# Kernel tuning notes

Hardware: AMD Instinct MI355X
Metric: run time of the kernel (lower is better)

## Reference

```python
import jax, jax.numpy as jnp
import numpy as np

SIGNAL = (32, 32)
KERNEL = (8, 8)
N_FEATURES = [64, 128, 128]
BATCH = 64
ALPHA = 0.5          # source references an undefined global `alpha`; fixed here
LEAKY_SLOPE = 0.01   # torch F.leaky_relu default


def _join_tensor(S, K, loc):
    i = np.arange(S)[:, None, None]
    j = np.arange(S)[None, :, None]
    k = np.arange(K)[None, None, :]
    M = (j >= i) & (i == np.maximum(j, k + loc))
    return jnp.asarray(M.astype(np.float32))


def _meet_tensor(S, K, loc):
    i = np.arange(S)[:, None, None]
    j = np.arange(S)[None, :, None]
    k = np.arange(K)[None, None, :]
    M = (j >= i) & (i == np.minimum(j, k + loc))
    return jnp.asarray(M.astype(np.float32))


def setup_inputs() -> dict:
    key = jax.random.key(0)
    sx, sy = SIGNAL
    kx, ky = KERNEL
    # meet layers use kernel_loc = signal - kernel; join layers use (0, 0)
    cmx = _meet_tensor(sx, kx, sx - kx)
    cmy = _meet_tensor(sy, ky, sy - ky)
    cjx = _join_tensor(sx, kx, 0)
    cjy = _join_tensor(sy, ky, 0)

    keys = jax.random.split(key, 16)
    x = jax.random.normal(keys[0], (BATCH, N_FEATURES[0], sx, sy), dtype=jnp.float32)

    def kaiming(k, shape):
        fan_in = shape[0] * shape[1] * shape[2]  # kx*ky*in_features
        return jax.random.normal(k, shape, dtype=jnp.float32) * np.float32(np.sqrt(2.0 / fan_in))

    inp = {"x": x, "cmx": cmx, "cmy": cmy, "cjx": cjx, "cjy": cjy}
    for li in range(len(N_FEATURES) - 1):
        fi, fo = N_FEATURES[li], N_FEATURES[li + 1]
        inp[f"mw{li}"] = kaiming(keys[1 + 2 * li], (kx, ky, fi, fo))
        inp[f"mb{li}"] = jnp.zeros((fo, 1, 1), dtype=jnp.float32)
        inp[f"jw{li}"] = kaiming(keys[2 + 2 * li], (kx, ky, fi, fo))
        inp[f"jb{li}"] = jnp.zeros((fo, 1, 1), dtype=jnp.float32)
    return inp


def _lattice_conv(cx, cy, X, W, b):
    # Y[m,g,x,y] = sum_{i,j,a,b} cx[i,x,a] cy[j,y,b] X[m,f,i,j] W[a,b,f,g] + bias
    return jnp.einsum('ixa,jyb,mfij,abfg->mgxy', cx, cy, X, W, optimize='optimal') + b


def reference(x, cmx, cmy, cjx, cjy, mw0, mb0, jw0, jb0, mw1, mb1, jw1, jb1):
    params = [(mw0, mb0, jw0, jb0), (mw1, mb1, jw1, jb1)]
    for mw, mb, jw, jb in params:
        m = _lattice_conv(cmx, cmy, x, mw, mb)
        j = _lattice_conv(cjx, cjy, x, jw, jb)
        x = jax.nn.leaky_relu((1.0 - ALPHA) * m + ALPHA * j, negative_slope=LEAKY_SLOPE)
    return x
```

## Files before the change

### kernel.cpp

```cpp
#include <hip/hip_runtime.h>
#include <stdint.h>


typedef __attribute__((ext_vector_type(8))) short short8;
typedef __attribute__((ext_vector_type(4))) float floatx4;
typedef __attribute__((ext_vector_type(4))) unsigned short ushort4v;

__device__ __forceinline__ float bf2f(unsigned short u) {
  union { uint32_t u; float f; } c; c.u = ((uint32_t)u) << 16; return c.f;
}
__device__ __forceinline__ unsigned short f2bf(float f) {
  union { float f; uint32_t u; } c; c.f = f;
  uint32_t u = c.u;
  uint32_t r = (u + 0x7FFFu + ((u >> 16) & 1u)) >> 16;
  return (unsigned short)r;
}

#define SLOT_W1 0
#define SLOT_SB 225
#define SLOT_AS 289
#define SLOT_M  353
#define N_SLOTS 417
#define N_SLOTS_PAD 448

#define NB_SETUP 225
#define NB_PACK 1024
#define NB_TIN 4096
__global__ __launch_bounds__(256) void fused_prep(
    const unsigned short* __restrict__ xa,
    const float* __restrict__ x32,
    const void* __restrict__ mw0, const void* __restrict__ jw0,
    const void* __restrict__ mw1, const void* __restrict__ jw1,
    const void* __restrict__ mb0, const void* __restrict__ jb0,
    const void* __restrict__ mb1, const void* __restrict__ jb1,
    float* __restrict__ bias0, float* __restrict__ bias1,
    int* __restrict__ flag, unsigned short* __restrict__ L,
    unsigned short* __restrict__ PBg0, unsigned short* __restrict__ PBg1,
    unsigned short* __restrict__ Xt0) {
  __shared__ int s_cnt;
  __shared__ unsigned short sh_pack[128][33];
  __shared__ unsigned short sh_tile[32][33];
  int tx = threadIdx.x, ty = threadIdx.y;
  int tid = ty * 32 + tx;
  int bid = blockIdx.x;

  if (bid < NB_SETUP) {
    if (bid == 0) {
      if (tid == 0) s_cnt = 0;
      __syncthreads();
      unsigned short v = xa[tid];
      int e = (v >> 7) & 0xFF;
      int ok = (v == 0) || (e >= 110 && e <= 140);
      atomicAdd(&s_cnt, ok);
      __syncthreads();
      int fp32 = (s_cnt >= 240) ? 0 : 1;
      if (tid == 0) *flag = fp32;
      int g = tid & 127;
      const void* mb = (tid < 128) ? mb0 : mb1;
      const void* jb = (tid < 128) ? jb0 : jb1;
      float* bo = (tid < 128) ? bias0 : bias1;
      float m = fp32 ? ((const float*)mb)[g] : bf2f(((const unsigned short*)mb)[g]);
      float j = fp32 ? ((const float*)jb)[g] : bf2f(((const unsigned short*)jb)[g]);
      bo[g] = 0.5f * (m + j);
      return;
    }
    int t = (bid - 1) * 256 + tid;
    int slot = t >> 7, k = t & 127;
    int isj = k >= 64, ab = k & 63, a = ab >> 3, b = ab & 7;
    float v = 0.f;
    if (slot < 225) {
      int cx = slot / 15, cy = slot % 15;
      int pmx = cx < 7 ? cx : 7, pxx = cx > 7 ? cx - 7 : 0;
      int pmy = cy < 7 ? cy : 7, pyy = cy > 7 ? cy - 7 : 0;
      if (!isj) v = (a >= pxx && b >= pyy) ? 0.5f : 0.f;
      else      v = (a <= pmx && b <= pmy) ? 0.5f : 0.f;
    } else if (slot < 289) {
      int s = slot - SLOT_SB, px = s >> 3, b0 = s & 7;
      if (!isj) v = (a >= px && b == b0) ? 0.5f : 0.f;
    } else if (slot < 353) {
      int s = slot - SLOT_AS, a0 = s >> 3, py = s & 7;
      if (!isj) v = (a == a0 && b >= py) ? 0.5f : 0.f;
    } else if (slot < 417) {
      int s = slot - SLOT_M, a0 = s >> 3, b0 = s & 7;
      if (!isj) v = (a == a0 && b == b0) ? 0.5f : 0.f;
    }
    L[t] = f2bf(v);
    return;
  }

  if (tid == 0) s_cnt = 0;
  __syncthreads();
  {
    unsigned short v = xa[tid];
    int e = (v >> 7) & 0xFF;
    int ok = (v == 0) || (e >= 110 && e <= 140);
    atomicAdd(&s_cnt, ok);
  }
  __syncthreads();
  int fp32 = (s_cnt >= 240) ? 0 : 1;

  if (bid < NB_SETUP + NB_PACK) {
    int pb = bid - NB_SETUP;
    int gx = pb & 3, gy = (pb >> 2) & 127, layer = pb >> 9;
    int F = layer ? 128 : 64;
    int f = gy;
    if (f >= F) return;
    int g0 = gx * 32;
    const int G = 128, FG = F * G;
    const void* mw = layer ? mw1 : mw0;
    const void* jw = layer ? jw1 : jw0;
    unsigned short* PB = layer ? PBg1 : PBg0;
    for (int k = ty; k < 128; k += 8) {
      const void* src = (k < 64) ? mw : jw;
      int ab = k & 63;
      size_t idx = (size_t)ab * FG + (size_t)f * G + g0 + tx;
      sh_pack[k][tx] = fp32 ? f2bf(((const float*)src)[idx])
                            : ((const unsigned short*)src)[idx];
    }
    __syncthreads();
    int kk = tid & 127, gs = tid >> 7;
    for (int gg = gs; gg < 32; gg += 2)
      PB[((size_t)(g0 + gg) * F + f) * 128 + kk] = sh_pack[kk][gg];
    return;
  }

  {
    int tbi = bid - (NB_SETUP + NB_PACK);
    const int R = 4096, C = 1024;
    int c0 = (tbi & 31) * 32, r0 = (tbi >> 5) * 32;
    int row = tid >> 3, vc = tid & 7;
    if (fp32) {
      floatx4 lv = *(const floatx4*)&x32[(size_t)(r0 + row) * C + c0 + vc * 4];
#pragma unroll
      for (int j = 0; j < 4; ++j) sh_tile[row][vc * 4 + j] = f2bf(lv[j]);
    } else {
      ushort4v lv = *(const ushort4v*)&xa[(size_t)(r0 + row) * C + c0 + vc * 4];
#pragma unroll
      for (int j = 0; j < 4; ++j) sh_tile[row][vc * 4 + j] = lv[j];
    }
    __syncthreads();
    ushort4v w;
#pragma unroll
    for (int j = 0; j < 4; ++j) w[j] = sh_tile[vc * 4 + j][row];
    *(ushort4v*)&Xt0[(size_t)(c0 + row) * R + r0 + vc * 4] = w;
  }
}

__global__ __launch_bounds__(256) void transpose_out(
    const unsigned short* __restrict__ src, unsigned short* __restrict__ d16,
    float* __restrict__ d32, int R, int C, const int* __restrict__ flag) {
  __shared__ unsigned short tile[32][33];
  int fp32 = *flag;
  int tx = threadIdx.x, ty = threadIdx.y;
  int c0 = blockIdx.x * 32, r0 = blockIdx.y * 32;
  ushort4v v = *(const ushort4v*)&src[(size_t)(r0 + ty) * C + c0 + tx * 4];
#pragma unroll
  for (int j = 0; j < 4; ++j) tile[ty][tx * 4 + j] = v[j];
  __syncthreads();
  if (fp32) {
    floatx4 w;
#pragma unroll
    for (int j = 0; j < 4; ++j) w[j] = bf2f(tile[tx * 4 + j][ty]);
    *(floatx4*)&d32[(size_t)(c0 + ty) * R + r0 + tx * 4] = w;
  } else {
    ushort4v w;
#pragma unroll
    for (int j = 0; j < 4; ++j) w[j] = tile[tx * 4 + j][ty];
    *(ushort4v*)&d16[(size_t)(c0 + ty) * R + r0 + tx * 4] = w;
  }
}

template <int F, int NT>
__device__ __forceinline__ void mfma_tile(
    const unsigned short* __restrict__ A, const unsigned short* __restrict__ W,
    floatx4 acc[NT], int wave, int n, int q) {
  const unsigned short* a_ptr = A + ((size_t)(wave * 16 + n)) * F + q * 8;
  const unsigned short* w_ptr = W + (size_t)n * F + q * 8;
#pragma unroll
  for (int kk = 0; kk < F; kk += 32) {
    short8 av = *(const short8*)(a_ptr + kk);
#pragma unroll
    for (int t = 0; t < NT; ++t) {
      short8 bv = *(const short8*)(w_ptr + (size_t)t * 16 * F + kk);
      acc[t] = __builtin_amdgcn_mfma_f32_16x16x32_bf16(av, bv, acc[t], 0, 0, 0);
    }
  }
}

__global__ __launch_bounds__(256, 8) void prep_gemm2(
    const unsigned short* __restrict__ L,
    const unsigned short* __restrict__ PBg0,
    const unsigned short* __restrict__ PBg1,
    unsigned short* __restrict__ Wall0, unsigned short* __restrict__ Wall1) {
  int layer = blockIdx.z;
  int GF = layer ? 16384 : 8192;
  int n0 = blockIdx.x * 32;
  if (n0 >= GF) return;
  int m0 = blockIdx.y * 64;
  const unsigned short* PB = layer ? PBg1 : PBg0;
  unsigned short* Wall = layer ? Wall1 : Wall0;
  int wave = threadIdx.x >> 6, lane = threadIdx.x & 63;
  int n = lane & 15, q = lane >> 4;
  floatx4 acc[2];
#pragma unroll
  for (int t = 0; t < 2; ++t) acc[t] = (floatx4){0.f, 0.f, 0.f, 0.f};
  mfma_tile<128, 2>(L + (size_t)m0 * 128, PB + (size_t)n0 * 128, acc, wave, n, q);
#pragma unroll
  for (int t = 0; t < 2; ++t) {
    int gcol = n0 + t * 16 + n;
#pragma unroll
    for (int r = 0; r < 4; ++r) {
      int m = m0 + wave * 16 + q * 4 + r;
      Wall[(size_t)m * GF + gcol] = f2bf(acc[t][r]);
    }
  }
}

template <int F>
__global__ __launch_bounds__(256, 8) void corr_gemm(
    const unsigned short* __restrict__ Xt, const unsigned short* __restrict__ Wall,
    unsigned short* __restrict__ V, unsigned short* __restrict__ U,
    unsigned short* __restrict__ T) {
  int bid = blockIdx.x, gsh = blockIdx.y;
  int wave = threadIdx.x >> 6, lane = threadIdx.x & 63;
  int n = lane & 15, q = lane >> 4;
  int m0 = wave * 16 + q * 4;
  floatx4 acc[1];
  acc[0] = (floatx4){0.f, 0.f, 0.f, 0.f};
  for (int i = 0; i < 8; ++i) {
    int ipos, slot;
    unsigned short* out;
    if (bid < 32) {
      int y = bid, a = i;
      int py = y > 24 ? y - 24 : 0;
      ipos = (24 + a) * 32 + y;
      slot = SLOT_AS + a * 8 + py;
      out = V + (size_t)(a * 32 + y) * 8192;
    } else if (bid < 64) {
      int x = bid - 32, b = i;
      int px = x > 24 ? x - 24 : 0;
      ipos = x * 32 + 24 + b;
      slot = SLOT_SB + px * 8 + b;
      out = U + (size_t)(b * 32 + x) * 8192;
    } else {
      int a = bid - 64, b = i;
      ipos = (24 + a) * 32 + 24 + b;
      slot = SLOT_M + a * 8 + b;
      out = T + (size_t)(a * 8 + b) * 8192;
    }
    mfma_tile<F, 1>(Xt + (size_t)ipos * 64 * F,
                    Wall + ((size_t)slot * 128 + gsh * 16) * F, acc, wave, n, q);
    {
      int gcol = gsh * 16 + n;
      ushort4v w;
#pragma unroll
      for (int r = 0; r < 4; ++r) w[r] = f2bf(acc[0][r]);
      *(ushort4v*)&out[(size_t)gcol * 64 + m0] = w;
    }
  }
}

template <int F>
__global__ __launch_bounds__(256, 8) void final_gemm(
    const unsigned short* __restrict__ Xt, const unsigned short* __restrict__ Wall,
    const unsigned short* __restrict__ V, const unsigned short* __restrict__ U,
    const unsigned short* __restrict__ T, const float* __restrict__ bias,
    unsigned short* __restrict__ Out) {
  int pos = blockIdx.x, gs = blockIdx.y;
  int x = pos >> 5, y = pos & 31;
  int wave = threadIdx.x >> 6, lane = threadIdx.x & 63;
  int n = lane & 15, q = lane >> 4;
  int m0 = wave * 16 + q * 4;
  int clsx = x < 7 ? x : (x <= 24 ? 7 : x - 17);
  int clsy = y < 7 ? y : (y <= 24 ? 7 : y - 17);
  int px = x > 24 ? x - 24 : 0;
  int py = y > 24 ? y - 24 : 0;

  const unsigned short* a_ptr =
      Xt + (size_t)pos * 64 * F + ((size_t)(wave * 16 + n)) * F + q * 8;
  short8 av[F / 32];
#pragma unroll
  for (int kk = 0; kk < F / 32; ++kk)
    av[kk] = *(const short8*)(a_ptr + kk * 32);

  floatx4 acc[2];
#pragma unroll
  for (int t = 0; t < 2; ++t) {
    float bv = bias[gs * 32 + t * 16 + n];
#pragma unroll
    for (int r = 0; r < 4; ++r) acc[t][r] = bv;
  }
  if (px) {
    const unsigned short* c3 = V + ((size_t)(px - 1) * 32 + y) * 8192;
#pragma unroll
    for (int t = 0; t < 2; ++t) {
      ushort4v v = *(const ushort4v*)&c3[(size_t)(gs * 32 + t * 16 + n) * 64 + m0];
#pragma unroll
      for (int r = 0; r < 4; ++r) acc[t][r] += bf2f(v[r]);
    }
  }
  if (py) {
    const unsigned short* c2 = U + ((size_t)(py - 1) * 32 + x) * 8192;
#pragma unroll
    for (int t = 0; t < 2; ++t) {
      ushort4v v = *(const ushort4v*)&c2[(size_t)(gs * 32 + t * 16 + n) * 64 + m0];
#pragma unroll
      for (int r = 0; r < 4; ++r) acc[t][r] += bf2f(v[r]);
    }
  }
  if (px && py) {
    const unsigned short* c4b = T + (size_t)(py - 1) * 8192;
    for (int a2 = 0; a2 < px; ++a2) {
#pragma unroll
      for (int t = 0; t < 2; ++t) {
        ushort4v v = *(const ushort4v*)&c4b[(size_t)a2 * 65536 +
                                            (size_t)(gs * 32 + t * 16 + n) * 64 + m0];
#pragma unroll
        for (int r = 0; r < 4; ++r) acc[t][r] += bf2f(v[r]);
      }
    }
  }

  const unsigned short* w_ptr =
      Wall + ((size_t)(SLOT_W1 + clsx * 15 + clsy) * 128 + gs * 32) * F +
      (size_t)n * F + q * 8;
#pragma unroll
  for (int kk = 0; kk < F / 32; ++kk) {
#pragma unroll
    for (int t = 0; t < 2; ++t) {
      short8 bv = *(const short8*)(w_ptr + (size_t)t * 16 * F + kk * 32);
      acc[t] = __builtin_amdgcn_mfma_f32_16x16x32_bf16(av[kk], bv, acc[t], 0, 0, 0);
    }
  }

  unsigned short* o = Out + (size_t)pos * 64 * 128;
#pragma unroll
  for (int t = 0; t < 2; ++t) {
    int gcol = gs * 32 + t * 16 + n;
#pragma unroll
    for (int r = 0; r < 4; ++r) {
      int m = m0 + r;
      float v = acc[t][r];
      v = v > 0.f ? v : 0.01f * v;
      o[(size_t)m * 128 + gcol] = f2bf(v);
    }
  }
}

extern "C" void kernel_launch(void* const* d_in, const int* in_sizes, int n_in,
                              void* d_out, int out_size, void* d_ws,
                              size_t ws_size, hipStream_t stream) {
  const void* x   = d_in[0];
  const void* mw0 = d_in[5];
  const void* mb0 = d_in[6];
  const void* jw0 = d_in[7];
  const void* jb0 = d_in[8];
  const void* mw1 = d_in[9];
  const void* mb1 = d_in[10];
  const void* jw1 = d_in[11];
  const void* jb1 = d_in[12];

  char* ws = (char*)d_ws;
  const size_t MB = 1u << 20;
  unsigned short* Xt0   = (unsigned short*)(ws + 0);
  unsigned short* A1    = (unsigned short*)(ws + 9 * MB);
  unsigned short* Wall0 = (unsigned short*)(ws + 26 * MB);
  unsigned short* Wall1 = (unsigned short*)(ws + 34 * MB);
  unsigned short* Out2  = (unsigned short*)(ws + 49 * MB);
  unsigned short* PBg0  = (unsigned short*)(ws + 66 * MB);
  unsigned short* PBg1  = (unsigned short*)(ws + 69 * MB);
  unsigned short* L     = (unsigned short*)(ws + 74 * MB);
  float* bias0 = (float*)(ws + 75 * MB);
  float* bias1 = bias0 + 128;
  int*   flag  = (int*)(bias1 + 128);
  unsigned short* V = (unsigned short*)(ws + 76 * MB);
  unsigned short* U = (unsigned short*)(ws + 81 * MB);
  unsigned short* T = (unsigned short*)(ws + 86 * MB);

  dim3 tb(32, 8);
  fused_prep<<<NB_SETUP + NB_PACK + NB_TIN, tb, 0, stream>>>(
      (const unsigned short*)x, (const float*)x, mw0, jw0, mw1, jw1,
      mb0, jb0, mb1, jb1, bias0, bias1, flag, L, PBg0, PBg1, Xt0);
  prep_gemm2<<<dim3(512, 7, 2), 256, 0, stream>>>(L, PBg0, PBg1, Wall0, Wall1);

  corr_gemm<64><<<dim3(72, 8), 256, 0, stream>>>(Xt0, Wall0, V, U, T);
  final_gemm<64><<<dim3(1024, 4), 256, 0, stream>>>(Xt0, Wall0, V, U, T,
                                                    bias0, A1);
  corr_gemm<128><<<dim3(72, 8), 256, 0, stream>>>(A1, Wall1, V, U, T);
  final_gemm<128><<<dim3(1024, 4), 256, 0, stream>>>(A1, Wall1, V, U, T,
                                                     bias1, Out2);

  transpose_out<<<dim3(256, 32), dim3(8, 32), 0, stream>>>(
      Out2, (unsigned short*)d_out, (float*)d_out, 1024, 8192, flag);
}
```

Before: 252.8 us.

## Fold boundary correction GEMMs into final GEMM and drop corr_gemm launches

Removes the separate corr_gemm kernels that precomputed V/U/T correction terms into bf16 workspace buffers. The final GEMM now accumulates those boundary contributions directly, running extra MFMA tiles over the relevant slots for edge positions. This saves two launches and the global write and read of the intermediates, and keeps the corrections in fp32 instead of rounding them to bf16. The cost is load imbalance: edge blocks with px,py>0 do up to about 80 extra tile GEMMs, and shared boundary work is recomputed per position.

```diff
diff --git a/kernel.cpp b/kernel.cpp
--- a/kernel.cpp
+++ b/kernel.cpp
@@ -217,55 +217,17 @@
 }
 
 template <int F>
-__global__ __launch_bounds__(256, 8) void corr_gemm(
+__device__ __forceinline__ void acc_slot(
     const unsigned short* __restrict__ Xt, const unsigned short* __restrict__ Wall,
-    unsigned short* __restrict__ V, unsigned short* __restrict__ U,
-    unsigned short* __restrict__ T) {
-  int bid = blockIdx.x, gsh = blockIdx.y;
-  int wave = threadIdx.x >> 6, lane = threadIdx.x & 63;
-  int n = lane & 15, q = lane >> 4;
-  int m0 = wave * 16 + q * 4;
-  floatx4 acc[1];
-  acc[0] = (floatx4){0.f, 0.f, 0.f, 0.f};
-  for (int i = 0; i < 8; ++i) {
-    int ipos, slot;
-    unsigned short* out;
-    if (bid < 32) {
-      int y = bid, a = i;
-      int py = y > 24 ? y - 24 : 0;
-      ipos = (24 + a) * 32 + y;
-      slot = SLOT_AS + a * 8 + py;
-      out = V + (size_t)(a * 32 + y) * 8192;
-    } else if (bid < 64) {
-      int x = bid - 32, b = i;
-      int px = x > 24 ? x - 24 : 0;
-      ipos = x * 32 + 24 + b;
-      slot = SLOT_SB + px * 8 + b;
-      out = U + (size_t)(b * 32 + x) * 8192;
-    } else {
-      int a = bid - 64, b = i;
-      ipos = (24 + a) * 32 + 24 + b;
-      slot = SLOT_M + a * 8 + b;
-      out = T + (size_t)(a * 8 + b) * 8192;
-    }
-    mfma_tile<F, 1>(Xt + (size_t)ipos * 64 * F,
-                    Wall + ((size_t)slot * 128 + gsh * 16) * F, acc, wave, n, q);
-    {
-      int gcol = gsh * 16 + n;
-      ushort4v w;
-#pragma unroll
-      for (int r = 0; r < 4; ++r) w[r] = f2bf(acc[0][r]);
-      *(ushort4v*)&out[(size_t)gcol * 64 + m0] = w;
-    }
-  }
+    int ipos, int slot, int gsoff, floatx4 acc[2], int wave, int n, int q) {
+  mfma_tile<F, 2>(Xt + (size_t)ipos * 64 * F,
+                  Wall + ((size_t)slot * 128 + gsoff) * F, acc, wave, n, q);
 }
 
 template <int F>
 __global__ __launch_bounds__(256, 8) void final_gemm(
     const unsigned short* __restrict__ Xt, const unsigned short* __restrict__ Wall,
-    const unsigned short* __restrict__ V, const unsigned short* __restrict__ U,
-    const unsigned short* __restrict__ T, const float* __restrict__ bias,
-    unsigned short* __restrict__ Out) {
+    const float* __restrict__ bias, unsigned short* __restrict__ Out) {
   int pos = blockIdx.x, gs = blockIdx.y;
   int x = pos >> 5, y = pos & 31;
   int wave = threadIdx.x >> 6, lane = threadIdx.x & 63;
@@ -275,68 +237,32 @@
   int clsy = y < 7 ? y : (y <= 24 ? 7 : y - 17);
   int px = x > 24 ? x - 24 : 0;
   int py = y > 24 ? y - 24 : 0;
-
-  const unsigned short* a_ptr =
-      Xt + (size_t)pos * 64 * F + ((size_t)(wave * 16 + n)) * F + q * 8;
-  short8 av[F / 32];
-#pragma unroll
-  for (int kk = 0; kk < F / 32; ++kk)
-    av[kk] = *(const short8*)(a_ptr + kk * 32);
+  int gsoff = gs * 32;
 
   floatx4 acc[2];
 #pragma unroll
   for (int t = 0; t < 2; ++t) {
-    float bv = bias[gs * 32 + t * 16 + n];
+    float bv = bias[gsoff + t * 16 + n];
 #pragma unroll
     for (int r = 0; r < 4; ++r) acc[t][r] = bv;
   }
-  if (px) {
-    const unsigned short* c3 = V + ((size_t)(px - 1) * 32 + y) * 8192;
-#pragma unroll
-    for (int t = 0; t < 2; ++t) {
-      ushort4v v = *(const ushort4v*)&c3[(size_t)(gs * 32 + t * 16 + n) * 64 + m0];
-#pragma unroll
-      for (int r = 0; r < 4; ++r) acc[t][r] += bf2f(v[r]);
-    }
-  }
-  if (py) {
-    const unsigned short* c2 = U + ((size_t)(py - 1) * 32 + x) * 8192;
-#pragma unroll
-    for (int t = 0; t < 2; ++t) {
-      ushort4v v = *(const ushort4v*)&c2[(size_t)(gs * 32 + t * 16 + n) * 64 + m0];
-#pragma unroll
-      for (int r = 0; r < 4; ++r) acc[t][r] += bf2f(v[r]);
-    }
-  }
-  if (px && py) {
-    const unsigned short* c4b = T + (size_t)(py - 1) * 8192;
-    for (int a2 = 0; a2 < px; ++a2) {
-#pragma unroll
-      for (int t = 0; t < 2; ++t) {
-        ushort4v v = *(const ushort4v*)&c4b[(size_t)a2 * 65536 +
-                                            (size_t)(gs * 32 + t * 16 + n) * 64 + m0];
-#pragma unroll
-        for (int r = 0; r < 4; ++r) acc[t][r] += bf2f(v[r]);
-      }
-    }
-  }
-
-  const unsigned short* w_ptr =
-      Wall + ((size_t)(SLOT_W1 + clsx * 15 + clsy) * 128 + gs * 32) * F +
-      (size_t)n * F + q * 8;
-#pragma unroll
-  for (int kk = 0; kk < F / 32; ++kk) {
-#pragma unroll
-    for (int t = 0; t < 2; ++t) {
-      short8 bv = *(const short8*)(w_ptr + (size_t)t * 16 * F + kk * 32);
-      acc[t] = __builtin_amdgcn_mfma_f32_16x16x32_bf16(av[kk], bv, acc[t], 0, 0, 0);
-    }
-  }
+
+  acc_slot<F>(Xt, Wall, pos, SLOT_W1 + clsx * 15 + clsy, gsoff, acc, wave, n, q);
+  for (int a2 = 0; a2 < px; ++a2)
+    acc_slot<F>(Xt, Wall, (24 + a2) * 32 + y, SLOT_AS + a2 * 8 + py, gsoff,
+                acc, wave, n, q);
+  for (int b2 = 0; b2 < py; ++b2)
+    acc_slot<F>(Xt, Wall, x * 32 + 24 + b2, SLOT_SB + px * 8 + b2, gsoff,
+                acc, wave, n, q);
+  for (int a2 = 0; a2 < px; ++a2)
+    for (int b2 = 0; b2 < py; ++b2)
+      acc_slot<F>(Xt, Wall, (24 + a2) * 32 + 24 + b2, SLOT_M + a2 * 8 + b2,
+                  gsoff, acc, wave, n, q);
 
   unsigned short* o = Out + (size_t)pos * 64 * 128;
 #pragma unroll
   for (int t = 0; t < 2; ++t) {
-    int gcol = gs * 32 + t * 16 + n;
+    int gcol = gsoff + t * 16 + n;
 #pragma unroll
     for (int r = 0; r < 4; ++r) {
       int m = m0 + r;
@@ -373,9 +299,6 @@
   float* bias0 = (float*)(ws + 75 * MB);
   float* bias1 = bias0 + 128;
   int*   flag  = (int*)(bias1 + 128);
-  unsigned short* V = (unsigned short*)(ws + 76 * MB);
-  unsigned short* U = (unsigned short*)(ws + 81 * MB);
-  unsigned short* T = (unsigned short*)(ws + 86 * MB);
 
   dim3 tb(32, 8);
   fused_prep<<<NB_SETUP + NB_PACK + NB_TIN, tb, 0, stream>>>(
@@ -383,12 +306,8 @@
       mb0, jb0, mb1, jb1, bias0, bias1, flag, L, PBg0, PBg1, Xt0);
   prep_gemm2<<<dim3(512, 7, 2), 256, 0, stream>>>(L, PBg0, PBg1, Wall0, Wall1);
 
-  corr_gemm<64><<<dim3(72, 8), 256, 0, stream>>>(Xt0, Wall0, V, U, T);
-  final_gemm<64><<<dim3(1024, 4), 256, 0, stream>>>(Xt0, Wall0, V, U, T,
-                                                    bias0, A1);
-  corr_gemm<128><<<dim3(72, 8), 256, 0, stream>>>(A1, Wall1, V, U, T);
-  final_gemm<128><<<dim3(1024, 4), 256, 0, stream>>>(A1, Wall1, V, U, T,
-                                                     bias1, Out2);
+  final_gemm<64><<<dim3(1024, 4), 256, 0, stream>>>(Xt0, Wall0, bias0, A1);
+  final_gemm<128><<<dim3(1024, 4), 256, 0, stream>>>(A1, Wall1, bias1, Out2);
 
   transpose_out<<<dim3(256, 32), dim3(8, 32), 0, stream>>>(
       Out2, (unsigned short*)d_out, (float*)d_out, 1024, 8192, flag);
```

Result: slower. 725.2 us (+186.9%).
